# Kernel optimization log

Hardware: AMD Instinct MI355X
Metric: run time of the kernel (lower is better)

The kernel has to match this reference:

```python
import jax, jax.numpy as jnp
import numpy as np

N, E, D_IN, D_H, G = 20000, 320000, 512, 256, 128


def setup_inputs() -> dict:
    key = jax.random.key(0)
    ks = jax.random.split(key, 9)
    x = jax.random.normal(ks[0], (N, D_IN), dtype=jnp.float32)
    edge_index = jax.random.randint(ks[1], (2, E), 0, N, dtype=jnp.int32)
    batch = jnp.sort(jax.random.randint(ks[2], (N,), 0, G, dtype=jnp.int32))
    W1 = jax.random.normal(ks[3], (D_IN, D_H), dtype=jnp.float32) / np.float32(np.sqrt(D_IN))
    b1 = jnp.zeros((D_H,), dtype=jnp.float32)
    W2 = jax.random.normal(ks[4], (D_H, D_H), dtype=jnp.float32) / np.float32(np.sqrt(D_H))
    b2 = jnp.zeros((D_H,), dtype=jnp.float32)
    w_fc = jax.random.normal(ks[5], (D_H, 1), dtype=jnp.float32) / np.float32(np.sqrt(D_H))
    b_fc = jnp.zeros((1,), dtype=jnp.float32)
    return {"x": x, "edge_index": edge_index, "batch": batch,
            "W1": W1, "b1": b1, "W2": W2, "b2": b2, "w_fc": w_fc, "b_fc": b_fc}


def gcn_conv(x, W, b, src, dst, n):
    # PyG GCNConv: out = D^{-1/2} (A+I) D^{-1/2} (X W) + b  (self-loops already in src/dst)
    xw = x @ W                                            # [n, d_out]
    deg = jnp.zeros((n,), xw.dtype).at[dst].add(1.0)       # in-degree incl. self loop
    dinv = jnp.where(deg > 0, jax.lax.rsqrt(deg), 0.0)
    coef = (dinv[src] * dinv[dst])[:, None]               # [e, 1]
    out = jnp.zeros_like(xw).at[dst].add(xw[src] * coef)  # gather-scale-scatter
    return out + b


def reference(x, edge_index, batch, W1, b1, W2, b2, w_fc, b_fc):
    n = x.shape[0]
    loops = jnp.arange(n, dtype=edge_index.dtype)
    src = jnp.concatenate([edge_index[0], loops])
    dst = jnp.concatenate([edge_index[1], loops])
    h = jax.nn.relu(gcn_conv(x, W1, b1, src, dst, n))
    h = jax.nn.relu(gcn_conv(h, W2, b2, src, dst, n))
    # global_mean_pool over graph ids
    sums = jax.ops.segment_sum(h, batch, num_segments=G)                      # [G, d]
    cnt = jax.ops.segment_sum(jnp.ones((n, 1), h.dtype), batch, num_segments=G)
    pooled = sums / jnp.maximum(cnt, 1.0)
    return (pooled @ w_fc + b_fc)[:, 0]                                       # [G]
```

## Files before the change

### kernel.cpp

```cpp
#include <hip/hip_runtime.h>
#include <hip/hip_fp16.h>


#define TPB 256
#define CAP 64

typedef _Float16 hfrag __attribute__((ext_vector_type(8)));
typedef float f32x4 __attribute__((ext_vector_type(4)));
typedef float f32x8 __attribute__((ext_vector_type(8)));

__global__ __launch_bounds__(TPB) void k_init(int* __restrict__ cursor, int N,
                                              const float* __restrict__ W1,
                                              unsigned short* __restrict__ B1, int K1,
                                              const float* __restrict__ W2,
                                              unsigned short* __restrict__ B2, int K2) {
  int nbz = (N + TPB - 1) / TPB;
  int b = blockIdx.x;
  if (b < nbz) {
    int i = b * TPB + threadIdx.x;
    if (i < N) cursor[i] = 0;
    return;
  }
  int t = (b - nbz) * TPB + threadIdx.x;
  const float* W = W1;
  unsigned short* B = B1;
  if (t >= K1 * 256) {
    t -= K1 * 256;
    if (t >= K2 * 256) return;
    W = W2; B = B2;
  }
  int n = t & 255, k = t >> 8;
  __half h = __float2half(W[(size_t)k * 256 + n]);
  B[((size_t)(k >> 5) * 256 + n) * 32 + (k & 31)] = *(unsigned short*)&h;
}

#define LDSTR 72

template <int MODE>
__device__ __forceinline__ void gemm_core(const unsigned short* __restrict__ Bp,
                                          __half* __restrict__ C, int M, int K,
                                          int bm, int bn,
                                          unsigned short (*As)[LDSTR],
                                          const float* A_f32,
                                          const __half* A_f16) {
  const int tid = threadIdx.x;
  const int w = tid >> 6;
  const int lane = tid & 63;
  const int q = lane >> 4;
  const int nin = lane & 15;
  const int r  = tid >> 2;
  const int cb = (tid & 3) << 4;
  const int row = bm + r;
  const bool rok = row < M;

  size_t bbase[2];
#pragma unroll
  for (int nt = 0; nt < 2; ++nt)
    bbase[nt] = ((size_t)(bn + w * 32 + nt * 16 + nin)) * 32 + q * 8;

  f32x4 acc[4][2];
#pragma unroll
  for (int mt = 0; mt < 4; ++mt)
#pragma unroll
    for (int nt = 0; nt < 2; ++nt) acc[mt][nt] = (f32x4){0.f, 0.f, 0.f, 0.f};

  float4 rf[4];
  uint4  rh[2];
  if (MODE == 0) {
    rf[0] = make_float4(0.f, 0.f, 0.f, 0.f); rf[1] = rf[0]; rf[2] = rf[0]; rf[3] = rf[0];
    if (rok) {
      const float* Ap = A_f32 + (size_t)row * K + cb;
      rf[0] = *(const float4*)(Ap);
      rf[1] = *(const float4*)(Ap + 4);
      rf[2] = *(const float4*)(Ap + 8);
      rf[3] = *(const float4*)(Ap + 12);
    }
  } else {
    rh[0] = make_uint4(0, 0, 0, 0); rh[1] = rh[0];
    if (rok) {
      const __half* Ap = A_f16 + (size_t)row * K + cb;
      rh[0] = *(const uint4*)(Ap);
      rh[1] = *(const uint4*)(Ap + 8);
    }
  }

  for (int kb = 0; kb < K; kb += 64) {
    if (MODE == 0) {
      float vv[16];
      *(float4*)&vv[0] = rf[0]; *(float4*)&vv[4] = rf[1];
      *(float4*)&vv[8] = rf[2]; *(float4*)&vv[12] = rf[3];
      unsigned short h16[16];
#pragma unroll
      for (int j = 0; j < 16; ++j) {
        __half h = __float2half(vv[j]);
        h16[j] = *(unsigned short*)&h;
      }
      __syncthreads();
      *(uint4*)&As[r][cb]     = *(uint4*)&h16[0];
      *(uint4*)&As[r][cb + 8] = *(uint4*)&h16[8];
      __syncthreads();
    } else {
      __syncthreads();
      *(uint4*)&As[r][cb]     = rh[0];
      *(uint4*)&As[r][cb + 8] = rh[1];
      __syncthreads();
    }

    int kn = kb + 64;
    if (kn < K && rok) {
      if (MODE == 0) {
        const float* Ap = A_f32 + (size_t)row * K + kn + cb;
        rf[0] = *(const float4*)(Ap);
        rf[1] = *(const float4*)(Ap + 4);
        rf[2] = *(const float4*)(Ap + 8);
        rf[3] = *(const float4*)(Ap + 12);
      } else {
        const __half* Ap = A_f16 + (size_t)row * K + kn + cb;
        rh[0] = *(const uint4*)(Ap);
        rh[1] = *(const uint4*)(Ap + 8);
      }
    }

#pragma unroll
    for (int s = 0; s < 2; ++s) {
      const size_t koff = (size_t)((kb >> 5) + s) * 256 * 32;
      hfrag bf[2];
#pragma unroll
      for (int nt = 0; nt < 2; ++nt)
        bf[nt] = *(const hfrag*)(Bp + koff + bbase[nt]);
      hfrag af[4];
#pragma unroll
      for (int mt = 0; mt < 4; ++mt)
        af[mt] = *(const hfrag*)&As[mt * 16 + nin][s * 32 + q * 8];
#pragma unroll
      for (int mt = 0; mt < 4; ++mt)
#pragma unroll
        for (int nt = 0; nt < 2; ++nt)
          acc[mt][nt] = __builtin_amdgcn_mfma_f32_16x16x32_f16(af[mt], bf[nt], acc[mt][nt], 0, 0, 0);
    }
  }

#pragma unroll
  for (int mt = 0; mt < 4; ++mt) {
    int rb = bm + mt * 16 + q * 4;
#pragma unroll
    for (int reg = 0; reg < 4; ++reg) {
      int rr = rb + reg;
      if (rr < M) {
#pragma unroll
        for (int nt = 0; nt < 2; ++nt)
          C[(size_t)rr * 256 + bn + w * 32 + nt * 16 + nin] = __float2half(acc[mt][nt][reg]);
      }
    }
  }
}

__global__ __launch_bounds__(TPB) void k_gemm1_scatter(const float* __restrict__ A,
                                                       const unsigned short* __restrict__ Bp,
                                                       __half* __restrict__ C, int M, int K,
                                                       const int* __restrict__ src,
                                                       const int* __restrict__ dst,
                                                       int* __restrict__ cursor,
                                                       unsigned* __restrict__ pairw, int E) {
  __shared__ unsigned short As[64][LDSTR];
  int nbg = 2 * ((M + 63) / 64);
  int b = blockIdx.x;
  if (b < nbg) {
    gemm_core<0>(Bp, C, M, K, (b >> 1) * 64, (b & 1) * 128, As, A, nullptr);
    return;
  }
  int e = (b - nbg) * TPB + threadIdx.x;
  if (e >= E) return;
  int s = src[e], d = dst[e];
  int pos = d * CAP + atomicAdd(&cursor[d], 1);
  pairw[pos] = (unsigned)s;
}

__global__ __launch_bounds__(TPB) void k_gemm2(const __half* __restrict__ A,
                                               const unsigned short* __restrict__ Bp,
                                               __half* __restrict__ C, int M, int K) {
  __shared__ unsigned short As[64][LDSTR];
  gemm_core<1>(Bp, C, M, K, blockIdx.y * 64, blockIdx.x * 128, As, nullptr, A);
}

__device__ __forceinline__ void fma8(f32x8& a, float coef, uint4 v) {
  float2 f0 = __half22float2(*(__half2*)&v.x);
  float2 f1 = __half22float2(*(__half2*)&v.y);
  float2 f2 = __half22float2(*(__half2*)&v.z);
  float2 f3 = __half22float2(*(__half2*)&v.w);
  a[0] = fmaf(coef, f0.x, a[0]);
  a[1] = fmaf(coef, f0.y, a[1]);
  a[2] = fmaf(coef, f1.x, a[2]);
  a[3] = fmaf(coef, f1.y, a[3]);
  a[4] = fmaf(coef, f2.x, a[4]);
  a[5] = fmaf(coef, f2.y, a[5]);
  a[6] = fmaf(coef, f3.x, a[6]);
  a[7] = fmaf(coef, f3.y, a[7]);
}

__global__ __launch_bounds__(TPB) void k_gather1(const uint4* __restrict__ xq4,
                                                 const int* __restrict__ cnt,
                                                 unsigned* __restrict__ pairw,
                                                 const float* __restrict__ bias,
                                                 uint4* __restrict__ h1, int N) {
  int node = __builtin_amdgcn_readfirstlane(blockIdx.x * 4 + (threadIdx.x >> 6));
  if (node >= N) return;
  int deg = __builtin_amdgcn_readfirstlane(cnt[node]);
  int lane = threadIdx.x & 63;
  int half = lane >> 5, li = lane & 31;
  int base = node * CAP;
  float ci = (float)(deg + 1);

  f32x8 a = (f32x8){0.f, 0.f, 0.f, 0.f, 0.f, 0.f, 0.f, 0.f};
  int k = 0;
  for (; k + 7 < deg; k += 8) {
#pragma unroll
    for (int u = 0; u < 8; u += 2) {
      int j = (int)pairw[base + k + u + half];
      float coef = rsqrtf(ci * (float)(cnt[j] + 1));
      uint4 v = xq4[((size_t)j << 5) + li];
      fma8(a, coef, v);
    }
  }
  for (; k < deg; k += 2) {
    int kk = k + half;
    int j = 0;
    float coef = 0.f;
    if (kk < deg) {
      j = (int)pairw[base + kk];
      coef = rsqrtf(ci * (float)(cnt[j] + 1));
    }
    uint4 v = xq4[((size_t)j << 5) + li];
    fma8(a, coef, v);
  }
#pragma unroll
  for (int i = 0; i < 8; ++i) a[i] += __shfl_xor(a[i], 32);

  float di2 = 1.f / ci;
  uint4 sv = xq4[((size_t)node << 5) + li];
  fma8(a, di2, sv);
  const float4 b0 = *(const float4*)&bias[8 * li];
  const float4 b1v = *(const float4*)&bias[8 * li + 4];
  float r0 = fmaxf(a[0] + b0.x, 0.f), r1 = fmaxf(a[1] + b0.y, 0.f);
  float r2 = fmaxf(a[2] + b0.z, 0.f), r3 = fmaxf(a[3] + b0.w, 0.f);
  float r4 = fmaxf(a[4] + b1v.x, 0.f), r5 = fmaxf(a[5] + b1v.y, 0.f);
  float r6 = fmaxf(a[6] + b1v.z, 0.f), r7 = fmaxf(a[7] + b1v.w, 0.f);
  if (half == 0) {
    __half2 o0 = __floats2half2_rn(r0, r1);
    __half2 o1 = __floats2half2_rn(r2, r3);
    __half2 o2 = __floats2half2_rn(r4, r5);
    __half2 o3 = __floats2half2_rn(r6, r7);
    uint4 o;
    o.x = *(unsigned*)&o0; o.y = *(unsigned*)&o1;
    o.z = *(unsigned*)&o2; o.w = *(unsigned*)&o3;
    h1[((size_t)node << 5) + li] = o;
  }

  if (lane < deg) {
    int j = (int)pairw[base + lane];
    float coef = rsqrtf(ci * (float)(cnt[j] + 1));
    __half hc = __float2half(coef);
    pairw[base + lane] = ((unsigned)j << 16) | (unsigned)(*(unsigned short*)&hc);
  }
}

__global__ __launch_bounds__(TPB) void k_gather2(const uint4* __restrict__ xq4,
                                                 const int* __restrict__ cnt,
                                                 const unsigned* __restrict__ pairw,
                                                 const float* __restrict__ bias,
                                                 const float* __restrict__ wfc,
                                                 float* __restrict__ pdot, int N) {
  int node = __builtin_amdgcn_readfirstlane(blockIdx.x * 4 + (threadIdx.x >> 6));
  if (node >= N) return;
  int deg = __builtin_amdgcn_readfirstlane(cnt[node]);
  int lane = threadIdx.x & 63;
  int half = lane >> 5, li = lane & 31;
  int base = node * CAP;

  f32x8 a = (f32x8){0.f, 0.f, 0.f, 0.f, 0.f, 0.f, 0.f, 0.f};
  int k = 0;
  for (; k + 7 < deg; k += 8) {
#pragma unroll
    for (int u = 0; u < 8; u += 2) {
      unsigned uu = pairw[base + k + u + half];
      unsigned short cb16 = (unsigned short)(uu & 0xFFFFu);
      float coef = __half2float(*(__half*)&cb16);
      uint4 v = xq4[((size_t)(uu >> 16) << 5) + li];
      fma8(a, coef, v);
    }
  }
  for (; k < deg; k += 2) {
    int kk = k + half;
    unsigned uu = (kk < deg) ? pairw[base + kk] : 0u;
    unsigned short cb16 = (unsigned short)(uu & 0xFFFFu);
    float coef = (kk < deg) ? __half2float(*(__half*)&cb16) : 0.f;
    uint4 v = xq4[((size_t)(uu >> 16) << 5) + li];
    fma8(a, coef, v);
  }
#pragma unroll
  for (int i = 0; i < 8; ++i) a[i] += __shfl_xor(a[i], 32);

  float di2 = 1.f / (float)(deg + 1);
  uint4 sv = xq4[((size_t)node << 5) + li];
  fma8(a, di2, sv);
  const float4 b0 = *(const float4*)&bias[8 * li];
  const float4 b1v = *(const float4*)&bias[8 * li + 4];
  const float4 f0 = *(const float4*)&wfc[8 * li];
  const float4 f1 = *(const float4*)&wfc[8 * li + 4];
  float s = fmaxf(a[0] + b0.x, 0.f) * f0.x + fmaxf(a[1] + b0.y, 0.f) * f0.y +
            fmaxf(a[2] + b0.z, 0.f) * f0.z + fmaxf(a[3] + b0.w, 0.f) * f0.w +
            fmaxf(a[4] + b1v.x, 0.f) * f1.x + fmaxf(a[5] + b1v.y, 0.f) * f1.y +
            fmaxf(a[6] + b1v.z, 0.f) * f1.z + fmaxf(a[7] + b1v.w, 0.f) * f1.w;
#pragma unroll
  for (int off = 16; off > 0; off >>= 1) s += __shfl_down(s, off, 32);
  if (lane == 0) pdot[node] = s;
}

__global__ __launch_bounds__(TPB) void k_pool(const float* __restrict__ pdot,
                                              const int* __restrict__ batch,
                                              const float* __restrict__ bfc,
                                              float* __restrict__ out, int N) {
  int g = blockIdx.x;
  int lo = 0, hi = N;
  while (lo < hi) { int mid = (lo + hi) >> 1; if (batch[mid] < g) lo = mid + 1; else hi = mid; }
  int start = lo;
  hi = N;
  while (lo < hi) { int mid = (lo + hi) >> 1; if (batch[mid] < g + 1) lo = mid + 1; else hi = mid; }
  int end = lo;

  float s = 0.f;
  for (int i = start + threadIdx.x; i < end; i += TPB) s += pdot[i];
  __shared__ float red[4];
  int lane = threadIdx.x & 63, wave = threadIdx.x >> 6;
#pragma unroll
  for (int off = 32; off > 0; off >>= 1) s += __shfl_down(s, off);
  if (lane == 0) red[wave] = s;
  __syncthreads();
  if (threadIdx.x == 0) {
    float tot = red[0] + red[1] + red[2] + red[3];
    float c = (float)(end - start);
    out[g] = tot / fmaxf(c, 1.f) + bfc[0];
  }
}

extern "C" void kernel_launch(void* const* d_in, const int* in_sizes, int n_in,
                              void* d_out, int out_size, void* d_ws, size_t ws_size,
                              hipStream_t stream) {
  const float* x    = (const float*)d_in[0];
  const int*   eidx = (const int*)d_in[1];
  const int*   batch= (const int*)d_in[2];
  const float* W1   = (const float*)d_in[3];
  const float* b1   = (const float*)d_in[4];
  const float* W2   = (const float*)d_in[5];
  const float* b2   = (const float*)d_in[6];
  const float* wfc  = (const float*)d_in[7];
  const float* bfc  = (const float*)d_in[8];
  float* out = (float*)d_out;

  const int N  = in_sizes[2];
  const int E  = in_sizes[1] / 2;
  const int K1 = in_sizes[0] / N;
  const int G  = out_size;

  const int* srcp = eidx;
  const int* dstp = eidx + E;

  auto al16 = [](size_t v) { return (v + 15) & ~(size_t)15; };
  char* ws = (char*)d_ws;
  size_t off = 0;
  int*      cursor = (int*)(ws + off);         off = al16(off + (size_t)N * 4);
  unsigned* pairw  = (unsigned*)(ws + off);    off = al16(off + (size_t)N * CAP * 4);
  float*    pdot   = (float*)(ws + off);       off = al16(off + (size_t)N * 4);
  __half*   bufH   = (__half*)(ws + off);      off = al16(off + (size_t)N * 256 * 2);
  __half*   h1f    = (__half*)(ws + off);      off = al16(off + (size_t)N * 256 * 2);
  unsigned short* W1h = (unsigned short*)(ws + off); off = al16(off + (size_t)K1 * 256 * 2);
  unsigned short* W2h = (unsigned short*)(ws + off); off = al16(off + (size_t)256 * 256 * 2);

  const int nbz = (N + TPB - 1) / TPB;
  const int nbW = ((K1 + 256) * 256 + TPB - 1) / TPB;
  const int nbE = (E + TPB - 1) / TPB;
  const int nbg = 2 * ((N + 63) / 64);
  const int nbG = (N + 3) / 4;
  const dim3 g2(2, (N + 63) / 64);

  k_init<<<nbz + nbW, TPB, 0, stream>>>(cursor, N, W1, W1h, K1, W2, W2h, 256);

  k_gemm1_scatter<<<nbg + nbE, TPB, 0, stream>>>(x, W1h, bufH, N, K1,
                                                 srcp, dstp, cursor, pairw, E);
  k_gather1<<<nbG, TPB, 0, stream>>>((const uint4*)bufH, cursor, pairw, b1,
                                     (uint4*)h1f, N);

  k_gemm2<<<g2, TPB, 0, stream>>>(h1f, W2h, bufH, N, 256);

  k_gather2<<<nbG, TPB, 0, stream>>>((const uint4*)bufH, cursor, pairw, b2,
                                     wfc, pdot, N);

  k_pool<<<G, TPB, 0, stream>>>(pdot, batch, bfc, out, N);
}
```

Before: 184.6 us.

## Store GEMM outputs as FP8 and gather with quarter-wave neighbor parallelism

The GEMM epilogues now write XW as FP8 (e4m3 via cvt_pk_fp8) instead of FP16, halving the bytes read by the edge gather kernels. Each gather wave now splits into four 16-lane groups that each process one neighbor, and neighbor indices and coefficients are broadcast from a register via shuffles instead of reloaded from memory. The W2 conversion moves from the init kernel into the gemm1/scatter launch. FP8 storage loses accuracy in the aggregated features, which may threaten tolerance, and the wider per-lane fragments add more reduction shuffles.

New measurement: 172.5 us. 6.5% less time.

```diff
diff --git a/kernel.cpp b/kernel.cpp
--- a/kernel.cpp
+++ b/kernel.cpp
@@ -7,13 +7,11 @@
 
 typedef _Float16 hfrag __attribute__((ext_vector_type(8)));
 typedef float f32x4 __attribute__((ext_vector_type(4)));
-typedef float f32x8 __attribute__((ext_vector_type(8)));
+typedef float f32x2 __attribute__((ext_vector_type(2)));
 
 __global__ __launch_bounds__(TPB) void k_init(int* __restrict__ cursor, int N,
                                               const float* __restrict__ W1,
-                                              unsigned short* __restrict__ B1, int K1,
-                                              const float* __restrict__ W2,
-                                              unsigned short* __restrict__ B2, int K2) {
+                                              unsigned short* __restrict__ B1, int K1) {
   int nbz = (N + TPB - 1) / TPB;
   int b = blockIdx.x;
   if (b < nbz) {
@@ -22,23 +20,17 @@
     return;
   }
   int t = (b - nbz) * TPB + threadIdx.x;
-  const float* W = W1;
-  unsigned short* B = B1;
-  if (t >= K1 * 256) {
-    t -= K1 * 256;
-    if (t >= K2 * 256) return;
-    W = W2; B = B2;
-  }
+  if (t >= K1 * 256) return;
   int n = t & 255, k = t >> 8;
-  __half h = __float2half(W[(size_t)k * 256 + n]);
-  B[((size_t)(k >> 5) * 256 + n) * 32 + (k & 31)] = *(unsigned short*)&h;
+  __half h = __float2half(W1[(size_t)k * 256 + n]);
+  B1[((size_t)(k >> 5) * 256 + n) * 32 + (k & 31)] = *(unsigned short*)&h;
 }
 
 #define LDSTR 72
 
 template <int MODE>
 __device__ __forceinline__ void gemm_core(const unsigned short* __restrict__ Bp,
-                                          __half* __restrict__ C, int M, int K,
+                                          unsigned char* __restrict__ C, int M, int K,
                                           int bm, int bn,
                                           unsigned short (*As)[LDSTR],
                                           const float* A_f32,
@@ -148,8 +140,11 @@
       int rr = rb + reg;
       if (rr < M) {
 #pragma unroll
-        for (int nt = 0; nt < 2; ++nt)
-          C[(size_t)rr * 256 + bn + w * 32 + nt * 16 + nin] = __float2half(acc[mt][nt][reg]);
+        for (int nt = 0; nt < 2; ++nt) {
+          float v = acc[mt][nt][reg];
+          int pk = __builtin_amdgcn_cvt_pk_fp8_f32(v, v, 0, false);
+          C[(size_t)rr * 256 + bn + w * 32 + nt * 16 + nin] = (unsigned char)(pk & 0xff);
+        }
       }
     }
   }
@@ -157,11 +152,13 @@
 
 __global__ __launch_bounds__(TPB) void k_gemm1_scatter(const float* __restrict__ A,
                                                        const unsigned short* __restrict__ Bp,
-                                                       __half* __restrict__ C, int M, int K,
+                                                       unsigned char* __restrict__ C, int M, int K,
                                                        const int* __restrict__ src,
                                                        const int* __restrict__ dst,
                                                        int* __restrict__ cursor,
-                                                       unsigned* __restrict__ pairw, int E) {
+                                                       unsigned* __restrict__ pairw, int E,
+                                                       const float* __restrict__ W2,
+                                                       unsigned short* __restrict__ W2h) {
   __shared__ unsigned short As[64][LDSTR];
   int nbg = 2 * ((M + 63) / 64);
   int b = blockIdx.x;
@@ -169,36 +166,66 @@
     gemm_core<0>(Bp, C, M, K, (b >> 1) * 64, (b & 1) * 128, As, A, nullptr);
     return;
   }
-  int e = (b - nbg) * TPB + threadIdx.x;
-  if (e >= E) return;
-  int s = src[e], d = dst[e];
-  int pos = d * CAP + atomicAdd(&cursor[d], 1);
-  pairw[pos] = (unsigned)s;
+  b -= nbg;
+  int nbE = (E + TPB - 1) / TPB;
+  if (b < nbE) {
+    int e = b * TPB + threadIdx.x;
+    if (e >= E) return;
+    int s = src[e], d = dst[e];
+    int pos = d * CAP + atomicAdd(&cursor[d], 1);
+    pairw[pos] = (unsigned)s;
+    return;
+  }
+  b -= nbE;
+  int t = b * TPB + threadIdx.x;
+  if (t >= 256 * 256) return;
+  int n = t & 255, k = t >> 8;
+  __half h = __float2half(W2[(size_t)k * 256 + n]);
+  W2h[((size_t)(k >> 5) * 256 + n) * 32 + (k & 31)] = *(unsigned short*)&h;
 }
 
 __global__ __launch_bounds__(TPB) void k_gemm2(const __half* __restrict__ A,
                                                const unsigned short* __restrict__ Bp,
-                                               __half* __restrict__ C, int M, int K) {
+                                               unsigned char* __restrict__ C, int M, int K) {
   __shared__ unsigned short As[64][LDSTR];
   gemm_core<1>(Bp, C, M, K, blockIdx.y * 64, blockIdx.x * 128, As, nullptr, A);
 }
 
-__device__ __forceinline__ void fma8(f32x8& a, float coef, uint4 v) {
-  float2 f0 = __half22float2(*(__half2*)&v.x);
-  float2 f1 = __half22float2(*(__half2*)&v.y);
-  float2 f2 = __half22float2(*(__half2*)&v.z);
-  float2 f3 = __half22float2(*(__half2*)&v.w);
-  a[0] = fmaf(coef, f0.x, a[0]);
-  a[1] = fmaf(coef, f0.y, a[1]);
-  a[2] = fmaf(coef, f1.x, a[2]);
-  a[3] = fmaf(coef, f1.y, a[3]);
-  a[4] = fmaf(coef, f2.x, a[4]);
-  a[5] = fmaf(coef, f2.y, a[5]);
-  a[6] = fmaf(coef, f3.x, a[6]);
-  a[7] = fmaf(coef, f3.y, a[7]);
-}
-
-__global__ __launch_bounds__(TPB) void k_gather1(const uint4* __restrict__ xq4,
+__device__ __forceinline__ void fma16(float* a, float coef, uint4 v) {
+#pragma unroll
+  for (int wv = 0; wv < 4; ++wv) {
+    unsigned word = (&v.x)[wv];
+    f32x2 lo = __builtin_amdgcn_cvt_pk_f32_fp8((int)word, false);
+    f32x2 hi = __builtin_amdgcn_cvt_pk_f32_fp8((int)word, true);
+    a[4 * wv + 0] = fmaf(coef, lo[0], a[4 * wv + 0]);
+    a[4 * wv + 1] = fmaf(coef, lo[1], a[4 * wv + 1]);
+    a[4 * wv + 2] = fmaf(coef, hi[0], a[4 * wv + 2]);
+    a[4 * wv + 3] = fmaf(coef, hi[1], a[4 * wv + 3]);
+  }
+}
+
+__device__ __forceinline__ void gather_loop(float* a, const uint4* __restrict__ xq,
+                                            unsigned wreg, int deg, int quarter, int li) {
+  int iters = (deg + 3) >> 2;
+  int itersP = (iters + 1) & ~1;
+  for (int p = 0; p < itersP; p += 2) {
+    int k0 = 4 * p + quarter, k1 = k0 + 4;
+    unsigned w0 = (unsigned)__shfl((int)wreg, k0);
+    unsigned w1 = (unsigned)__shfl((int)wreg, k1);
+    uint4 v0 = xq[((size_t)(w0 >> 16) << 4) + li];
+    uint4 v1 = xq[((size_t)(w1 >> 16) << 4) + li];
+    unsigned short c0 = (unsigned short)(w0 & 0xFFFFu);
+    unsigned short c1 = (unsigned short)(w1 & 0xFFFFu);
+    fma16(a, __half2float(*(__half*)&c0), v0);
+    fma16(a, __half2float(*(__half*)&c1), v1);
+  }
+#pragma unroll
+  for (int i = 0; i < 16; ++i) a[i] += __shfl_xor(a[i], 16);
+#pragma unroll
+  for (int i = 0; i < 16; ++i) a[i] += __shfl_xor(a[i], 32);
+}
+
+__global__ __launch_bounds__(TPB) void k_gather1(const uint4* __restrict__ xq,
                                                  const int* __restrict__ cnt,
                                                  unsigned* __restrict__ pairw,
                                                  const float* __restrict__ bias,
@@ -207,64 +234,54 @@
   if (node >= N) return;
   int deg = __builtin_amdgcn_readfirstlane(cnt[node]);
   int lane = threadIdx.x & 63;
-  int half = lane >> 5, li = lane & 31;
+  int quarter = lane >> 4, li = lane & 15;
   int base = node * CAP;
   float ci = (float)(deg + 1);
 
-  f32x8 a = (f32x8){0.f, 0.f, 0.f, 0.f, 0.f, 0.f, 0.f, 0.f};
-  int k = 0;
-  for (; k + 7 < deg; k += 8) {
-#pragma unroll
-    for (int u = 0; u < 8; u += 2) {
-      int j = (int)pairw[base + k + u + half];
-      float coef = rsqrtf(ci * (float)(cnt[j] + 1));
-      uint4 v = xq4[((size_t)j << 5) + li];
-      fma8(a, coef, v);
-    }
-  }
-  for (; k < deg; k += 2) {
-    int kk = k + half;
-    int j = 0;
-    float coef = 0.f;
-    if (kk < deg) {
-      j = (int)pairw[base + kk];
-      coef = rsqrtf(ci * (float)(cnt[j] + 1));
-    }
-    uint4 v = xq4[((size_t)j << 5) + li];
-    fma8(a, coef, v);
-  }
-#pragma unroll
-  for (int i = 0; i < 8; ++i) a[i] += __shfl_xor(a[i], 32);
-
-  float di2 = 1.f / ci;
-  uint4 sv = xq4[((size_t)node << 5) + li];
-  fma8(a, di2, sv);
-  const float4 b0 = *(const float4*)&bias[8 * li];
-  const float4 b1v = *(const float4*)&bias[8 * li + 4];
-  float r0 = fmaxf(a[0] + b0.x, 0.f), r1 = fmaxf(a[1] + b0.y, 0.f);
-  float r2 = fmaxf(a[2] + b0.z, 0.f), r3 = fmaxf(a[3] + b0.w, 0.f);
-  float r4 = fmaxf(a[4] + b1v.x, 0.f), r5 = fmaxf(a[5] + b1v.y, 0.f);
-  float r6 = fmaxf(a[6] + b1v.z, 0.f), r7 = fmaxf(a[7] + b1v.w, 0.f);
-  if (half == 0) {
-    __half2 o0 = __floats2half2_rn(r0, r1);
-    __half2 o1 = __floats2half2_rn(r2, r3);
-    __half2 o2 = __floats2half2_rn(r4, r5);
-    __half2 o3 = __floats2half2_rn(r6, r7);
-    uint4 o;
-    o.x = *(unsigned*)&o0; o.y = *(unsigned*)&o1;
-    o.z = *(unsigned*)&o2; o.w = *(unsigned*)&o3;
-    h1[((size_t)node << 5) + li] = o;
-  }
-
+  unsigned wreg = 0u;
   if (lane < deg) {
     int j = (int)pairw[base + lane];
-    float coef = rsqrtf(ci * (float)(cnt[j] + 1));
-    __half hc = __float2half(coef);
-    pairw[base + lane] = ((unsigned)j << 16) | (unsigned)(*(unsigned short*)&hc);
-  }
-}
-
-__global__ __launch_bounds__(TPB) void k_gather2(const uint4* __restrict__ xq4,
+    float c = rsqrtf(ci * (float)(cnt[j] + 1));
+    __half hc = __float2half(c);
+    wreg = ((unsigned)j << 16) | (unsigned)(*(unsigned short*)&hc);
+    pairw[base + lane] = wreg;
+  }
+
+  float a[16];
+#pragma unroll
+  for (int i = 0; i < 16; ++i) a[i] = 0.f;
+  gather_loop(a, xq, wreg, deg, quarter, li);
+
+  float di2 = 1.f / ci;
+  fma16(a, di2, xq[((size_t)node << 4) + li]);
+  if (quarter == 0) {
+    const float4 b0 = *(const float4*)&bias[16 * li];
+    const float4 b1v = *(const float4*)&bias[16 * li + 4];
+    const float4 b2v = *(const float4*)&bias[16 * li + 8];
+    const float4 b3v = *(const float4*)&bias[16 * li + 12];
+    float r[16];
+    r[0] = fmaxf(a[0] + b0.x, 0.f);  r[1] = fmaxf(a[1] + b0.y, 0.f);
+    r[2] = fmaxf(a[2] + b0.z, 0.f);  r[3] = fmaxf(a[3] + b0.w, 0.f);
+    r[4] = fmaxf(a[4] + b1v.x, 0.f); r[5] = fmaxf(a[5] + b1v.y, 0.f);
+    r[6] = fmaxf(a[6] + b1v.z, 0.f); r[7] = fmaxf(a[7] + b1v.w, 0.f);
+    r[8] = fmaxf(a[8] + b2v.x, 0.f); r[9] = fmaxf(a[9] + b2v.y, 0.f);
+    r[10] = fmaxf(a[10] + b2v.z, 0.f); r[11] = fmaxf(a[11] + b2v.w, 0.f);
+    r[12] = fmaxf(a[12] + b3v.x, 0.f); r[13] = fmaxf(a[13] + b3v.y, 0.f);
+    r[14] = fmaxf(a[14] + b3v.z, 0.f); r[15] = fmaxf(a[15] + b3v.w, 0.f);
+    unsigned o[8];
+#pragma unroll
+    for (int i = 0; i < 8; ++i) {
+      __half2 h2 = __floats2half2_rn(r[2 * i], r[2 * i + 1]);
+      o[i] = *(unsigned*)&h2;
+    }
+    uint4 o0 = make_uint4(o[0], o[1], o[2], o[3]);
+    uint4 o1 = make_uint4(o[4], o[5], o[6], o[7]);
+    h1[(size_t)node * 32 + 2 * li] = o0;
+    h1[(size_t)node * 32 + 2 * li + 1] = o1;
+  }
+}
+
+__global__ __launch_bounds__(TPB) void k_gather2(const uint4* __restrict__ xq,
                                                  const int* __restrict__ cnt,
                                                  const unsigned* __restrict__ pairw,
                                                  const float* __restrict__ bias,
@@ -274,45 +291,37 @@
   if (node >= N) return;
   int deg = __builtin_amdgcn_readfirstlane(cnt[node]);
   int lane = threadIdx.x & 63;
-  int half = lane >> 5, li = lane & 31;
+  int quarter = lane >> 4, li = lane & 15;
   int base = node * CAP;
 
-  f32x8 a = (f32x8){0.f, 0.f, 0.f, 0.f, 0.f, 0.f, 0.f, 0.f};
-  int k = 0;
-  for (; k + 7 < deg; k += 8) {
-#pragma unroll
-    for (int u = 0; u < 8; u += 2) {
-      unsigned uu = pairw[base + k + u + half];
-      unsigned short cb16 = (unsigned short)(uu & 0xFFFFu);
-      float coef = __half2float(*(__half*)&cb16);
-      uint4 v = xq4[((size_t)(uu >> 16) << 5) + li];
-      fma8(a, coef, v);
-    }
-  }
-  for (; k < deg; k += 2) {
-    int kk = k + half;
-    unsigned uu = (kk < deg) ? pairw[base + kk] : 0u;
-    unsigned short cb16 = (unsigned short)(uu & 0xFFFFu);
-    float coef = (kk < deg) ? __half2float(*(__half*)&cb16) : 0.f;
-    uint4 v = xq4[((size_t)(uu >> 16) << 5) + li];
-    fma8(a, coef, v);
-  }
-#pragma unroll
-  for (int i = 0; i < 8; ++i) a[i] += __shfl_xor(a[i], 32);
+  unsigned wreg = (lane < deg) ? pairw[base + lane] : 0u;
+
+  float a[16];
+#pragma unroll
+  for (int i = 0; i < 16; ++i) a[i] = 0.f;
+  gather_loop(a, xq, wreg, deg, quarter, li);
 
   float di2 = 1.f / (float)(deg + 1);
-  uint4 sv = xq4[((size_t)node << 5) + li];
-  fma8(a, di2, sv);
-  const float4 b0 = *(const float4*)&bias[8 * li];
-  const float4 b1v = *(const float4*)&bias[8 * li + 4];
-  const float4 f0 = *(const float4*)&wfc[8 * li];
-  const float4 f1 = *(const float4*)&wfc[8 * li + 4];
+  fma16(a, di2, xq[((size_t)node << 4) + li]);
+
+  const float4 b0 = *(const float4*)&bias[16 * li];
+  const float4 b1v = *(const float4*)&bias[16 * li + 4];
+  const float4 b2v = *(const float4*)&bias[16 * li + 8];
+  const float4 b3v = *(const float4*)&bias[16 * li + 12];
+  const float4 f0 = *(const float4*)&wfc[16 * li];
+  const float4 f1 = *(const float4*)&wfc[16 * li + 4];
+  const float4 f2 = *(const float4*)&wfc[16 * li + 8];
+  const float4 f3 = *(const float4*)&wfc[16 * li + 12];
   float s = fmaxf(a[0] + b0.x, 0.f) * f0.x + fmaxf(a[1] + b0.y, 0.f) * f0.y +
             fmaxf(a[2] + b0.z, 0.f) * f0.z + fmaxf(a[3] + b0.w, 0.f) * f0.w +
             fmaxf(a[4] + b1v.x, 0.f) * f1.x + fmaxf(a[5] + b1v.y, 0.f) * f1.y +
-            fmaxf(a[6] + b1v.z, 0.f) * f1.z + fmaxf(a[7] + b1v.w, 0.f) * f1.w;
-#pragma unroll
-  for (int off = 16; off > 0; off >>= 1) s += __shfl_down(s, off, 32);
+            fmaxf(a[6] + b1v.z, 0.f) * f1.z + fmaxf(a[7] + b1v.w, 0.f) * f1.w +
+            fmaxf(a[8] + b2v.x, 0.f) * f2.x + fmaxf(a[9] + b2v.y, 0.f) * f2.y +
+            fmaxf(a[10] + b2v.z, 0.f) * f2.z + fmaxf(a[11] + b2v.w, 0.f) * f2.w +
+            fmaxf(a[12] + b3v.x, 0.f) * f3.x + fmaxf(a[13] + b3v.y, 0.f) * f3.y +
+            fmaxf(a[14] + b3v.z, 0.f) * f3.z + fmaxf(a[15] + b3v.w, 0.f) * f3.w;
+#pragma unroll
+  for (int off = 8; off > 0; off >>= 1) s += __shfl_down(s, off, 16);
   if (lane == 0) pdot[node] = s;
 }
 
@@ -371,28 +380,30 @@
   int*      cursor = (int*)(ws + off);         off = al16(off + (size_t)N * 4);
   unsigned* pairw  = (unsigned*)(ws + off);    off = al16(off + (size_t)N * CAP * 4);
   float*    pdot   = (float*)(ws + off);       off = al16(off + (size_t)N * 4);
-  __half*   bufH   = (__half*)(ws + off);      off = al16(off + (size_t)N * 256 * 2);
+  unsigned char* bufQ = (unsigned char*)(ws + off); off = al16(off + (size_t)N * 256);
   __half*   h1f    = (__half*)(ws + off);      off = al16(off + (size_t)N * 256 * 2);
   unsigned short* W1h = (unsigned short*)(ws + off); off = al16(off + (size_t)K1 * 256 * 2);
   unsigned short* W2h = (unsigned short*)(ws + off); off = al16(off + (size_t)256 * 256 * 2);
 
-  const int nbz = (N + TPB - 1) / TPB;
-  const int nbW = ((K1 + 256) * 256 + TPB - 1) / TPB;
-  const int nbE = (E + TPB - 1) / TPB;
-  const int nbg = 2 * ((N + 63) / 64);
-  const int nbG = (N + 3) / 4;
+  const int nbz  = (N + TPB - 1) / TPB;
+  const int nbW1 = (K1 * 256 + TPB - 1) / TPB;
+  const int nbW2 = (256 * 256 + TPB - 1) / TPB;
+  const int nbE  = (E + TPB - 1) / TPB;
+  const int nbg  = 2 * ((N + 63) / 64);
+  const int nbG  = (N + 3) / 4;
   const dim3 g2(2, (N + 63) / 64);
 
-  k_init<<<nbz + nbW, TPB, 0, stream>>>(cursor, N, W1, W1h, K1, W2, W2h, 256);
-
-  k_gemm1_scatter<<<nbg + nbE, TPB, 0, stream>>>(x, W1h, bufH, N, K1,
-                                                 srcp, dstp, cursor, pairw, E);
-  k_gather1<<<nbG, TPB, 0, stream>>>((const uint4*)bufH, cursor, pairw, b1,
+  k_init<<<nbz + nbW1, TPB, 0, stream>>>(cursor, N, W1, W1h, K1);
+
+  k_gemm1_scatter<<<nbg + nbE + nbW2, TPB, 0, stream>>>(x, W1h, bufQ, N, K1,
+                                                        srcp, dstp, cursor, pairw, E,
+                                                        W2, W2h);
+  k_gather1<<<nbG, TPB, 0, stream>>>((const uint4*)bufQ, cursor, pairw, b1,
                                      (uint4*)h1f, N);
 
-  k_gemm2<<<g2, TPB, 0, stream>>>(h1f, W2h, bufH, N, 256);
-
-  k_gather2<<<nbG, TPB, 0, stream>>>((const uint4*)bufH, cursor, pairw, b2,
+  k_gemm2<<<g2, TPB, 0, stream>>>(h1f, W2h, bufQ, N, 256);
+
+  k_gather2<<<nbG, TPB, 0, stream>>>((const uint4*)bufQ, cursor, pairw, b2,
                                      wfc, pdot, N);
 
   k_pool<<<G, TPB, 0, stream>>>(pdot, batch, bfc, out, N);
```
